# Kernel tuning notes

Measured on AMD Instinct MI355X. Metric: run time of the kernel, lower is better.

The kernel has to match this reference:

```python
import jax, jax.numpy as jnp
import numpy as np

C = 1024
H = C // 64          # 16 heads
CH = 64              # head dim
NUM_BUCKETS = 32
MAX_DISTANCE = 64
REL_SCALE = float(np.sqrt(CH))  # (channels//num_heads)**0.5 = 8
EPS = 1e-5


def group_norm(x, gamma, beta, groups):
    # x: [B, C, T]
    B, Cc, T = x.shape
    xg = x.reshape(B, groups, -1)
    m = xg.mean(-1, keepdims=True)
    v = xg.var(-1, keepdims=True)
    xn = ((xg - m) * jax.lax.rsqrt(v + EPS)).reshape(B, Cc, T)
    return xn * gamma[None, :, None] + beta[None, :, None]


def conv1d(x, w, b, pad):
    # x: [B, Cin, T], w: [Cout, Cin, K]
    y = jax.lax.conv_general_dilated(x, w, (1,), [(pad, pad)],
                                     dimension_numbers=('NCH', 'OIH', 'NCH'))
    return y + b[None, :, None]


def rel_pos_bias(T, emb):
    # lucidrains RelativePositionBias, non-causal; emb: [num_buckets, H]
    pos = jnp.arange(T)
    n = pos[:, None] - pos[None, :]          # n = -(k - q) = q - k
    half = NUM_BUCKETS // 2                  # 16
    ret = (n < 0).astype(jnp.int32) * half
    n = jnp.abs(n)
    max_exact = half // 2                    # 8
    is_small = n < max_exact
    nf = jnp.maximum(n, 1).astype(jnp.float32)
    val_large = max_exact + (jnp.log(nf / max_exact)
                             / np.log(MAX_DISTANCE / max_exact)
                             * (half - max_exact)).astype(jnp.int32)
    val_large = jnp.minimum(val_large, half - 1)
    bucket = ret + jnp.where(is_small, n, val_large)  # [T, T]
    return emb[bucket].transpose(2, 0, 1)             # [H, T, T]


def setup_inputs() -> dict:
    key = jax.random.key(0)
    ks = jax.random.split(key, 20)
    B, T = 8, 1024
    s = 0.02
    return {
        'x': jax.random.normal(ks[0], (B, C, T), jnp.float32),
        # ResBlock in_layers
        'rb_gn1_g': jnp.ones((C,), jnp.float32),
        'rb_gn1_b': jnp.zeros((C,), jnp.float32),
        'rb_conv1_w': jax.random.normal(ks[1], (C, C, 3), jnp.float32) * s,
        'rb_conv1_b': jnp.zeros((C,), jnp.float32),
        # ResBlock out_layers (zero-init in original; randomized for testing)
        'rb_gn2_g': jnp.ones((C,), jnp.float32),
        'rb_gn2_b': jnp.zeros((C,), jnp.float32),
        'rb_conv2_w': jax.random.normal(ks[2], (C, C, 3), jnp.float32) * s,
        'rb_conv2_b': jnp.zeros((C,), jnp.float32),
        # outer GroupNorm(8, C)
        'norm_g': jnp.ones((C,), jnp.float32),
        'norm_b': jnp.zeros((C,), jnp.float32),
        # AttentionBlock
        'attn_gn_g': jnp.ones((C,), jnp.float32),
        'attn_gn_b': jnp.zeros((C,), jnp.float32),
        'qkv_w': jax.random.normal(ks[3], (3 * C, C, 1), jnp.float32) * s,
        'qkv_b': jnp.zeros((3 * C,), jnp.float32),
        'proj_w': jax.random.normal(ks[4], (C, C, 1), jnp.float32) * s,
        'proj_b': jnp.zeros((C,), jnp.float32),
        'rel_emb': jax.random.normal(ks[5], (NUM_BUCKETS, H), jnp.float32) * s,
    }


def reference(x, rb_gn1_g, rb_gn1_b, rb_conv1_w, rb_conv1_b,
              rb_gn2_g, rb_gn2_b, rb_conv2_w, rb_conv2_b,
              norm_g, norm_b, attn_gn_g, attn_gn_b,
              qkv_w, qkv_b, proj_w, proj_b, rel_emb):
    B, Cc, T = x.shape
    # ResBlock: GN32 -> SiLU -> conv3 -> GN32 -> SiLU -> (dropout=0) -> conv3, + skip
    h = jax.nn.silu(group_norm(x, rb_gn1_g, rb_gn1_b, 32))
    h = conv1d(h, rb_conv1_w, rb_conv1_b, 1)
    h = jax.nn.silu(group_norm(h, rb_gn2_g, rb_gn2_b, 32))
    h = conv1d(h, rb_conv2_w, rb_conv2_b, 1)
    h = x + h
    # outer GroupNorm(8)
    h = group_norm(h, norm_g, norm_b, 8)
    # AttentionBlock with relative position bias
    xin = h
    qkv = conv1d(group_norm(h, attn_gn_g, attn_gn_b, 32), qkv_w, qkv_b, 0)
    # channel layout after reshape(bs*H, 3*ch, T): [H, 3, ch]
    qkv = qkv.reshape(B, H, 3, CH, T)
    q, k, v = qkv[:, :, 0], qkv[:, :, 1], qkv[:, :, 2]
    scale = CH ** -0.25
    w = jnp.einsum('bhct,bhcs->bhts', q * scale, k * scale)
    bias = rel_pos_bias(T, rel_emb) * REL_SCALE       # [H, T, T]
    w = jax.nn.softmax((w + bias[None]).astype(jnp.float32), axis=-1).astype(w.dtype)
    a = jnp.einsum('bhts,bhcs->bhct', w, v).reshape(B, Cc, T)
    return xin + conv1d(a, proj_w, proj_b, 0)
```

## Files before the change

### kernel.cpp

```cpp
#include <hip/hip_runtime.h>

typedef __attribute__((ext_vector_type(4))) float f32x4;
typedef __attribute__((ext_vector_type(8))) __bf16 bf16x8;
typedef __attribute__((ext_vector_type(4))) unsigned short us4;
typedef __attribute__((ext_vector_type(8))) unsigned short us8;

#define DEVI static __device__ __forceinline__

DEVI unsigned short f2bf(float f){
  union { float f; unsigned u; } x; x.f = f;
  unsigned r = x.u + 0x7fffu + ((x.u >> 16) & 1u);
  return (unsigned short)(r >> 16);
}
DEVI float bf2f(unsigned short h){
  union { unsigned u; float f; } x; x.u = ((unsigned)h) << 16;
  return x.f;
}

typedef __attribute__((address_space(1))) unsigned int gu32;
typedef __attribute__((address_space(3))) unsigned int lu32;
DEVI void gll16(const void* g, void* l){
  __builtin_amdgcn_global_load_lds((gu32*)g, (lu32*)l, 16, 0, 0);
}

DEVI f32x4 mfma16(bf16x8 a, bf16x8 b, f32x4 c){
  return __builtin_amdgcn_mfma_f32_16x16x32_bf16(a, b, c, 0, 0, 0);
}

DEVI float wredsum(float v){
  #pragma unroll
  for (int m = 1; m < 64; m <<= 1) v += __shfl_xor(v, m);
  return v;
}

__global__ __launch_bounds__(256) void conv_w_prep2(const float* __restrict__ w1,
                                                    const float* __restrict__ w2,
                                                    unsigned short* __restrict__ wp1,
                                                    unsigned short* __restrict__ wp2){
  int idx = blockIdx.x * 256 + threadIdx.x;
  int sel = idx >> 20;
  int lo  = idx & 1048575;
  const float* p = (sel ? w2 : w1) + (size_t)lo * 3;
  unsigned short* wp = sel ? wp2 : wp1;
  wp[lo]           = f2bf(p[0]);
  wp[1048576 + lo] = f2bf(p[1]);
  wp[2097152 + lo] = f2bf(p[2]);
}

__global__ __launch_bounds__(256) void cast_f2b2(const float* __restrict__ qw,
                                                 const float* __restrict__ pw,
                                                 unsigned short* __restrict__ qo,
                                                 unsigned short* __restrict__ po){
  int idx = blockIdx.x * 256 + threadIdx.x;
  const float* src; unsigned short* dst; int lo;
  if (idx < 786432){ src = qw; dst = qo; lo = idx; }
  else             { src = pw; dst = po; lo = idx - 786432; }
  f32x4 v = *(const f32x4*)&src[(size_t)lo * 4];
  us4 o;
  #pragma unroll
  for (int j = 0; j < 4; j++) o[j] = f2bf(v[j]);
  *(us4*)&dst[(size_t)lo * 4] = o;
}

__global__ __launch_bounds__(256) void misc_prep(unsigned short* __restrict__ h1p,
                                                 unsigned short* __restrict__ g2p,
                                                 const float* __restrict__ emb,
                                                 float* __restrict__ btab){
  int bid = blockIdx.x;
  if (bid < 64){
    int idx = bid * 256 + threadIdx.x;
    int b = idx >> 11, rr = (idx >> 10) & 1, c = idx & 1023;
    size_t off = ((size_t)b * 1026 + (rr ? 1025 : 0)) * 1024 + c;
    h1p[off] = 0; g2p[off] = 0;
  } else {
    int idx = (bid - 64) * 256 + threadIdx.x;
    if (idx >= 2047 * 16) return;
    int d = idx >> 4, h = idx & 15;
    int n0 = d - 1023;
    int ret = (n0 < 0) ? 16 : 0;
    int n = (n0 < 0) ? -n0 : n0;
    int bucket;
    if (n < 8) bucket = ret + n;
    else {
      float ratio = logf((float)n * 0.125f) / 2.0794415416798357f;
      int vl = 8 + (int)(ratio * 8.0f);
      bucket = ret + (vl < 15 ? vl : 15);
    }
    btab[h * 2048 + d] = emb[bucket * 16 + h] * 11.541560327111707f;
  }
}

__global__ __launch_bounds__(256) void gn_stats_cast(const float* __restrict__ in,
                                                     float2* __restrict__ st,
                                                     unsigned short* __restrict__ xb){
  const int g = blockIdx.x; const int tid = threadIdx.x;
  const float* p = in + (size_t)g * 32768;
  unsigned short* q = xb + (size_t)g * 32768;
  float s = 0.f, s2 = 0.f;
  for (int i = tid * 4; i < 32768; i += 1024){
    f32x4 v = *(const f32x4*)&p[i];
    us4 o;
    #pragma unroll
    for (int j = 0; j < 4; j++){ s += v[j]; s2 += v[j] * v[j]; o[j] = f2bf(v[j]); }
    *(us4*)&q[i] = o;
  }
  s = wredsum(s); s2 = wredsum(s2);
  __shared__ float rs[4], rs2[4];
  if ((tid & 63) == 0){ rs[tid >> 6] = s; rs2[tid >> 6] = s2; }
  __syncthreads();
  if (tid == 0){
    float S = rs[0] + rs[1] + rs[2] + rs[3];
    float S2 = rs2[0] + rs2[1] + rs2[2] + rs2[3];
    float m = S * (1.f / 32768.f);
    float var = S2 * (1.f / 32768.f) - m * m;
    st[g] = make_float2(m, rsqrtf(var + 1e-5f));
  }
}

template<int SILU, int INBF16, int OUTPAD, int FROMPART>
__global__ __launch_bounds__(256) void gn_apply_tr(
    const void* __restrict__ inp, const float2* __restrict__ st,
    const float* __restrict__ gma, const float* __restrict__ bta,
    unsigned short* __restrict__ out)
{
  const int gid = blockIdx.x;
  const int tc = gid & 15, g = (gid >> 4) & 31, b = gid >> 9;
  const int tid = threadIdx.x;
  const int t0 = tc * 64;
  __shared__ __align__(16) unsigned short tr[64 * 40];
  float2 s;
  if (FROMPART){
    int g8 = g >> 2, k = g & 3;
    float S = 0.f, S2 = 0.f;
    #pragma unroll
    for (int j = 0; j < 4; j++){
      float2 v = st[(size_t)(b * 8 + g8) * 16 + k * 4 + j];
      S += v.x; S2 += v.y;
    }
    float m = S * (1.f / 32768.f);
    float var = S2 * (1.f / 32768.f) - m * m;
    s = make_float2(m, rsqrtf(var + 1e-5f));
  } else {
    s = st[b * 32 + g];
  }
  int c = tid >> 3, t8 = (tid & 7) * 8;
  int ch = g * 32 + c;
  float sc = gma[ch] * s.y;
  float sh = bta[ch] - s.x * sc;
  float vv[8];
  if (INBF16){
    const unsigned short* p = (const unsigned short*)inp + ((size_t)b * 1024 + ch) * 1024 + t0 + t8;
    us8 v = *(const us8*)p;
    #pragma unroll
    for (int j = 0; j < 8; j++) vv[j] = bf2f(v[j]);
  } else {
    const float* p = (const float*)inp + ((size_t)b * 1024 + ch) * 1024 + t0 + t8;
    f32x4 v0 = *(const f32x4*)p; f32x4 v1 = *(const f32x4*)(p + 4);
    #pragma unroll
    for (int j = 0; j < 4; j++){ vv[j] = v0[j]; vv[4 + j] = v1[j]; }
  }
  #pragma unroll
  for (int j = 0; j < 8; j++){
    float v = vv[j] * sc + sh;
    if (SILU) v = v / (1.f + __expf(-v));
    tr[(t8 + j) * 40 + c] = f2bf(v);
  }
  __syncthreads();
  int t = tid >> 2, c8 = (tid & 3) * 8;
  us8 d = *(const us8*)&tr[t * 40 + c8];
  size_t row = OUTPAD ? ((size_t)b * 1026 + 1 + t0 + t) : ((size_t)b * 1024 + t0 + t);
  *(us8*)&out[row * 1024 + g * 32 + c8] = d;
}

template<int SILU>
__global__ __launch_bounds__(256) void gn2_apply(const unsigned short* __restrict__ c1,
    const float2* __restrict__ part2, const float* __restrict__ gma, const float* __restrict__ bta,
    unsigned short* __restrict__ outp)
{
  const int tid = threadIdx.x;
  const int ck = blockIdx.x & 31, b = blockIdx.x >> 5;
  const int g = tid >> 3;
  float S = 0.f, S2 = 0.f;
  #pragma unroll
  for (int tt = 0; tt < 8; tt++){
    float2 v = part2[(size_t)(b * 8 + tt) * 32 + g];
    S += v.x; S2 += v.y;
  }
  float mm = S * (1.f / 32768.f);
  float var = S2 * (1.f / 32768.f) - mm * mm;
  float2 s = make_float2(mm, rsqrtf(var + 1e-5f));
  float sc[4], sh[4];
  #pragma unroll
  for (int j = 0; j < 4; j++){ int ch = tid * 4 + j; sc[j] = gma[ch] * s.y; sh[j] = bta[ch] - s.x * sc[j]; }
  const unsigned short* p = c1 + ((size_t)b * 1024 + ck * 32) * 1024 + tid * 4;
  unsigned short* q = outp + ((size_t)b * 1026 + 1 + ck * 32) * 1024 + tid * 4;
  for (int r = 0; r < 32; r++){
    us4 v = *(const us4*)&p[(size_t)r * 1024];
    us4 o;
    #pragma unroll
    for (int j = 0; j < 4; j++){
      float f = bf2f(v[j]) * sc[j] + sh[j];
      if (SILU) f = f / (1.f + __expf(-f));
      o[j] = f2bf(f);
    }
    *(us4*)&q[(size_t)r * 1024] = o;
  }
}

__global__ __launch_bounds__(256) void gn8_apply(const unsigned short* __restrict__ r,
    const float2* __restrict__ part8, const float* __restrict__ gma, const float* __restrict__ bta,
    unsigned short* __restrict__ xin, float2* __restrict__ part32){
  const int gid = blockIdx.x; const int tid = threadIdx.x;
  const int sub = gid & 15, g = (gid >> 4) & 7, b = gid >> 7;
  float S = 0.f, S2 = 0.f;
  #pragma unroll
  for (int tt = 0; tt < 8; tt++){
    float2 v = part8[(size_t)(b * 8 + tt) * 8 + g];
    S += v.x; S2 += v.y;
  }
  float mm = S * (1.f / 131072.f);
  float var = S2 * (1.f / 131072.f) - mm * mm;
  float2 s = make_float2(mm, rsqrtf(var + 1e-5f));
  const unsigned short* pr = r + ((size_t)(b * 8 + g)) * 131072 + sub * 8192;
  unsigned short* px = xin + ((size_t)(b * 8 + g)) * 131072 + sub * 8192;
  float ps = 0.f, ps2 = 0.f;
  for (int i = tid * 8; i < 8192; i += 2048){
    int c = g * 128 + sub * 8 + (i >> 10);
    float sc = gma[c] * s.y, sh = bta[c] - s.x * sc;
    us8 v = *(const us8*)&pr[i];
    us8 o;
    #pragma unroll
    for (int j = 0; j < 8; j++){
      float f = bf2f(v[j]) * sc + sh;
      ps += f; ps2 += f * f;
      o[j] = f2bf(f);
    }
    *(us8*)&px[i] = o;
  }
  ps = wredsum(ps); ps2 = wredsum(ps2);
  __shared__ float rs[4], rs2[4];
  if ((tid & 63) == 0){ rs[tid >> 6] = ps; rs2[tid >> 6] = ps2; }
  __syncthreads();
  if (tid == 0)
    part32[(size_t)(b * 8 + g) * 16 + sub] =
      make_float2(rs[0] + rs[1] + rs[2] + rs[3], rs2[0] + rs2[1] + rs2[2] + rs2[3]);
}

template<int KK, int EPI, int GPART>
__global__ __launch_bounds__(256, 2) void gemm_k(
    const unsigned short* __restrict__ inT,
    const unsigned short* __restrict__ W,
    const float* __restrict__ bias,
    void* __restrict__ outp,
    void* __restrict__ resp,
    float2* __restrict__ part,
    int OC, int NT)
{
  __shared__ __align__(16) unsigned short Alds[2][128 * 64];
  __shared__ __align__(16) unsigned short Blds[2][128 * 64];
  __shared__ float sred[16];
  const int tid = threadIdx.x;
  const int lane = tid & 63;
  const int w = tid >> 6;
  const int wn = w >> 1, wo = w & 1;
  const int nt = blockIdx.x % NT;
  const int ot = blockIdx.x / NT;
  const int b = nt >> 3;
  const int t0 = (nt & 7) * 128;
  const int ob = ot * 128;
  const int rowbase = (KK == 3) ? (b * 1026 + t0) : (b * 1024 + t0);
  const int NTI = KK * 16;

  f32x4 acc[4][4];
  #pragma unroll
  for (int m = 0; m < 4; m++)
    #pragma unroll
    for (int n = 0; n < 4; n++) acc[m][n] = 0.f;

  const int lrow = lane >> 3;
  const int lblk = lane & 7;

  auto stage = [&](int kt, int bufsel){
    int kk = kt >> 4;
    int i0 = (kt & 15) * 64;
    const unsigned short* Ab = inT + (size_t)(rowbase + kk) * 1024;
    const unsigned short* Bb = W + ((size_t)kk * OC + ob) * 1024;
    #pragma unroll
    for (int j = 0; j < 4; ++j){
      int chunk = w * 4 + j;
      int row = chunk * 8 + lrow;
      int gcol = (lblk ^ (row & 7)) * 8;
      gll16(Ab + (size_t)row * 1024 + i0 + gcol, &Alds[bufsel][chunk * 512]);
      gll16(Bb + (size_t)row * 1024 + i0 + gcol, &Blds[bufsel][chunk * 512]);
    }
  };

  stage(0, 0);
  stage(1, 1);
  asm volatile("s_waitcnt vmcnt(8)" ::: "memory");
  __builtin_amdgcn_sched_barrier(0);
  __builtin_amdgcn_s_barrier();
  __builtin_amdgcn_sched_barrier(0);

  #pragma unroll 2
  for (int kt = 0; kt < NTI; ++kt){
    const int cur = kt & 1;
    const unsigned short* Ab = &Alds[cur][0];
    const unsigned short* Bb = &Blds[cur][0];
    bf16x8 af[2][4], bfv[2][4];
    #pragma unroll
    for (int m = 0; m < 4; m++){
      int row = wn * 64 + m * 16 + (lane & 15);
      #pragma unroll
      for (int k2 = 0; k2 < 2; k2++){
        int blk = ((lane >> 4) + k2 * 4) ^ (row & 7);
        af[k2][m] = *(const bf16x8*)&Ab[row * 64 + blk * 8];
      }
    }
    #pragma unroll
    for (int n = 0; n < 4; n++){
      int row = wo * 64 + n * 16 + (lane & 15);
      #pragma unroll
      for (int k2 = 0; k2 < 2; k2++){
        int blk = ((lane >> 4) + k2 * 4) ^ (row & 7);
        bfv[k2][n] = *(const bf16x8*)&Bb[row * 64 + blk * 8];
      }
    }
    asm volatile("s_waitcnt lgkmcnt(0)" ::: "memory");
    __builtin_amdgcn_sched_barrier(0);
    __builtin_amdgcn_s_barrier();
    __builtin_amdgcn_sched_barrier(0);
    if (kt + 2 < NTI) stage(kt + 2, cur);
    __builtin_amdgcn_sched_barrier(0);
    __builtin_amdgcn_s_setprio(1);
    #pragma unroll
    for (int k2 = 0; k2 < 2; k2++)
      #pragma unroll
      for (int m = 0; m < 4; m++)
        #pragma unroll
        for (int n = 0; n < 4; n++)
          acc[m][n] = mfma16(af[k2][m], bfv[k2][n], acc[m][n]);
    __builtin_amdgcn_s_setprio(0);
    __builtin_amdgcn_sched_barrier(0);
    if (kt + 2 < NTI){ asm volatile("s_waitcnt vmcnt(8)" ::: "memory"); }
    else             { asm volatile("s_waitcnt vmcnt(0)" ::: "memory"); }
    __builtin_amdgcn_sched_barrier(0);
    __builtin_amdgcn_s_barrier();
    __builtin_amdgcn_sched_barrier(0);
  }

  if (EPI == 0){
    unsigned short* out = (unsigned short*)outp;
    float ps[2] = {0.f, 0.f}, ps2[2] = {0.f, 0.f};
    #pragma unroll
    for (int m = 0; m < 4; m++){
      int tl = t0 + wn * 64 + m * 16 + ((lane >> 4) * 4);
      #pragma unroll
      for (int n = 0; n < 4; n++){
        int o = ob + wo * 64 + n * 16 + (lane & 15);
        float bz = bias[o];
        size_t base = ((size_t)b * 1024 + tl) * OC + o;
        #pragma unroll
        for (int r = 0; r < 4; r++){
          float v = acc[m][n][r] + bz;
          if (GPART == 2){ ps[n >> 1] += v; ps2[n >> 1] += v * v; }
          out[base + (size_t)r * OC] = f2bf(v);
        }
      }
    }
    if (GPART == 2){
      #pragma unroll
      for (int j = 0; j < 2; j++){ ps[j] = wredsum(ps[j]); ps2[j] = wredsum(ps2[j]); }
      if (lane == 0){
        sred[w * 4 + 0] = ps[0]; sred[w * 4 + 1] = ps2[0];
        sred[w * 4 + 2] = ps[1]; sred[w * 4 + 3] = ps2[1];
      }
      __syncthreads();
      if (tid < 4){
        int g = tid, woo = g >> 1, jj = g & 1;
        float S  = sred[woo * 4 + jj * 2 + 0] + sred[(woo + 2) * 4 + jj * 2 + 0];
        float S2 = sred[woo * 4 + jj * 2 + 1] + sred[(woo + 2) * 4 + jj * 2 + 1];
        part[(size_t)(b * 8 + (nt & 7)) * 32 + ot * 4 + g] = make_float2(S, S2);
      }
    }
  } else if (EPI == 3){
    unsigned short* qkT = (unsigned short*)outp;
    unsigned short* vT  = (unsigned short*)resp;
    #pragma unroll
    for (int m = 0; m < 4; m++){
      int tl = t0 + wn * 64 + m * 16 + ((lane >> 4) * 4);
      #pragma unroll
      for (int n = 0; n < 4; n++){
        int o0 = ob + wo * 64 + n * 16;
        int h = o0 / 192;
        int rem0 = o0 - h * 192;
        int o = o0 + (lane & 15);
        float bz = bias[o];
        if (rem0 < 128){
          size_t base = ((size_t)b * 1024 + tl) * 2048 + h * 128 + rem0 + (lane & 15);
          #pragma unroll
          for (int r = 0; r < 4; r++)
            qkT[base + (size_t)r * 2048] = f2bf(acc[m][n][r] + bz);
        } else {
          int c = rem0 - 128 + (lane & 15);
          size_t base = (((size_t)(b * 16 + h)) * 64 + c) * 1024 + tl;
          us4 o4;
          #pragma unroll
          for (int r = 0; r < 4; r++) o4[r] = f2bf(acc[m][n][r] + bz);
          *(us4*)&vT[base] = o4;
        }
      }
    }
  } else if (EPI == 4){
    unsigned short* out = (unsigned short*)outp;
    const unsigned short* xr = (const unsigned short*)resp;
    float ps = 0.f, ps2 = 0.f;
    #pragma unroll
    for (int m = 0; m < 4; m++){
      int tl = t0 + wn * 64 + m * 16 + ((lane >> 4) * 4);
      #pragma unroll
      for (int n = 0; n < 4; n++){
        int o = ob + wo * 64 + n * 16 + (lane & 15);
        float bz = bias[o];
        size_t base = ((size_t)b * 1024 + o) * 1024 + tl;
        us4 xv = *(const us4*)&xr[base];
        us4 ov;
        #pragma unroll
        for (int r = 0; r < 4; r++){
          float v = bf2f(xv[r]) + acc[m][n][r] + bz;
          if (GPART == 8){ ps += v; ps2 += v * v; }
          ov[r] = f2bf(v);
        }
        *(us4*)&out[base] = ov;
      }
    }
    if (GPART == 8){
      ps = wredsum(ps); ps2 = wredsum(ps2);
      if (lane == 0){ sred[w * 2] = ps; sred[w * 2 + 1] = ps2; }
      __syncthreads();
      if (tid == 0){
        float S = sred[0] + sred[2] + sred[4] + sred[6];
        float S2 = sred[1] + sred[3] + sred[5] + sred[7];
        part[(size_t)(b * 8 + (nt & 7)) * 8 + ot] = make_float2(S, S2);
      }
    }
  } else {
    float* out = (float*)outp;
    #pragma unroll
    for (int m = 0; m < 4; m++){
      int tl = t0 + wn * 64 + m * 16 + ((lane >> 4) * 4);
      #pragma unroll
      for (int n = 0; n < 4; n++){
        int o = ob + wo * 64 + n * 16 + (lane & 15);
        float bz = bias[o];
        size_t base = ((size_t)b * 1024 + o) * 1024 + tl;
        const unsigned short* xr = (const unsigned short*)resp;
        us4 xv = *(const us4*)&xr[base];
        f32x4 v;
        v[0] = bf2f(xv[0]); v[1] = bf2f(xv[1]); v[2] = bf2f(xv[2]); v[3] = bf2f(xv[3]);
        #pragma unroll
        for (int r = 0; r < 4; r++) v[r] += acc[m][n][r] + bz;
        *(f32x4*)&out[base] = v;
      }
    }
  }
}

__global__ __launch_bounds__(256, 3) void attn_k9(
    const unsigned short* __restrict__ qkT,
    const unsigned short* __restrict__ vT,
    const float* __restrict__ btab,
    unsigned short* __restrict__ aT)
{
  __shared__ __align__(16) unsigned short Kb[2][64 * 64];
  __shared__ __align__(16) unsigned short Vb[2][64 * 64];
  __shared__ __align__(16) unsigned short Pb[4][32 * 64];
  __shared__ __align__(16) float cblds[288];
  const int tid = threadIdx.x, lane = tid & 63, w = tid >> 6;
  const int d0 = blockIdx.x;
  const int xcd = d0 & 7, slot = d0 >> 3;
  const int bh = xcd * 16 + (slot >> 3);
  const int qt = slot & 7;
  const int h = bh & 15, b = bh >> 4;
  const int q0b = qt * 128;
  const int q0 = q0b + w * 32;
  const unsigned short* qk = qkT + (size_t)b * 1024 * 2048 + h * 128;
  const unsigned short* vh = vT + ((size_t)(b * 16 + h)) * 64 * 1024;
  const int lc = lane & 15, lg = lane >> 4;

  const float bneg = btab[h * 2048 + 0];
  const float bpos = btab[h * 2048 + 2046];

  if (tid < 288) cblds[tid] = btab[h * 2048 + 879 + tid];

  bf16x8 qf[2][2];
  #pragma unroll
  for (int m = 0; m < 2; m++){
    const unsigned short* qrow = qk + (size_t)(q0 + m * 16 + lc) * 2048;
    #pragma unroll
    for (int k2 = 0; k2 < 2; k2++)
      qf[m][k2] = *(const bf16x8*)&qrow[k2 * 32 + lg * 8];
  }
  bf16x8 onesf;
  {
    us8 u;
    #pragma unroll
    for (int j = 0; j < 8; j++) u[j] = 0x3F80;
    onesf = *(bf16x8*)&u;
  }
  f32x4 oacc[2][4], lacc[2];
  #pragma unroll
  for (int m = 0; m < 2; m++){
    #pragma unroll
    for (int cb = 0; cb < 4; cb++) oacc[m][cb] = 0.f;
    lacc[m] = 0.f;
  }

  const int lr = lane >> 3, lb = lane & 7;
  const float qs = 0.18033688011112042f;

  #pragma unroll
  for (int j = 0; j < 2; j++){
    int chunk = w * 2 + j;
    int row = chunk * 8 + lr;
    int gcol = (lb ^ (row & 7)) * 8;
    gll16(qk + 64 + (size_t)row * 2048 + gcol, &Kb[0][chunk * 512]);
    gll16(vh + (size_t)row * 1024 + gcol, &Vb[0][chunk * 512]);
  }
  __syncthreads();

  for (int t = 0; t < 16; ++t){
    const int cur = t & 1;
    const int st0 = t * 64;
    if (t < 15){
      int nst = st0 + 64;
      #pragma unroll
      for (int j = 0; j < 2; j++){
        int chunk = w * 2 + j;
        int row = chunk * 8 + lr;
        int gcol = (lb ^ (row & 7)) * 8;
        gll16(qk + 64 + (size_t)(nst + row) * 2048 + gcol, &Kb[cur ^ 1][chunk * 512]);
        gll16(vh + (size_t)row * 1024 + nst + gcol, &Vb[cur ^ 1][chunk * 512]);
      }
    }
    f32x4 sfr[2][4];
    #pragma unroll
    for (int m = 0; m < 2; m++)
      #pragma unroll
      for (int sub = 0; sub < 4; sub++) sfr[m][sub] = 0.f;
    __builtin_amdgcn_s_setprio(1);
    #pragma unroll
    for (int sub = 0; sub < 4; sub++){
      int row = sub * 16 + lc;
      #pragma unroll
      for (int k2 = 0; k2 < 2; k2++){
        int blk = (lg + k2 * 4) ^ (row & 7);
        bf16x8 bk = *(const bf16x8*)&Kb[cur][row * 64 + blk * 8];
        sfr[0][sub] = mfma16(bk, qf[0][k2], sfr[0][sub]);
        sfr[1][sub] = mfma16(bk, qf[1][k2], sfr[1][sub]);
      }
    }
    __builtin_amdgcn_s_setprio(0);
    const bool unineg = (st0 >= q0 + 81);
    const bool unipos = (st0 + 113 <= q0);
    if (unineg || unipos){
      const float bc = unineg ? bneg : bpos;
      #pragma unroll
      for (int m = 0; m < 2; m++)
        #pragma unroll
        for (int sub = 0; sub < 4; sub++)
          #pragma unroll
          for (int r = 0; r < 4; r++)
            sfr[m][sub][r] = exp2f(fmaf(sfr[m][sub][r], qs, bc));
    } else {
      #pragma unroll
      for (int m = 0; m < 2; m++){
        const float* bp = &cblds[(q0 + m * 16 + lc) - st0 + 144 - lg * 4];
        #pragma unroll
        for (int sub = 0; sub < 4; sub++)
          #pragma unroll
          for (int r = 0; r < 4; r++)
            sfr[m][sub][r] = exp2f(fmaf(sfr[m][sub][r], qs, bp[-(sub * 16) - r]));
      }
    }
    unsigned short* P = &Pb[w][0];
    #pragma unroll
    for (int m = 0; m < 2; m++){
      int qrow = m * 16 + lc;
      int rsw = (qrow & 7) << 3;
      #pragma unroll
      for (int sub = 0; sub < 4; sub++){
        int col = sub * 16 + lg * 4;
        unsigned w0, w1;
        asm("v_cvt_pk_bf16_f32 %0, %1, %2" : "=v"(w0) : "v"(sfr[m][sub][0]), "v"(sfr[m][sub][1]));
        asm("v_cvt_pk_bf16_f32 %0, %1, %2" : "=v"(w1) : "v"(sfr[m][sub][2]), "v"(sfr[m][sub][3]));
        uint2 pk; pk.x = w0; pk.y = w1;
        *(uint2*)&P[qrow * 64 + (col ^ rsw)] = pk;
      }
    }
    __builtin_amdgcn_s_setprio(1);
    #pragma unroll
    for (int k2 = 0; k2 < 2; k2++){
      bf16x8 pa[2];
      #pragma unroll
      for (int m = 0; m < 2; m++){
        int rowp = m * 16 + lc;
        int blkp = (lg + k2 * 4) ^ (rowp & 7);
        pa[m] = *(const bf16x8*)&P[rowp * 64 + blkp * 8];
      }
      #pragma unroll
      for (int cb = 0; cb < 4; cb++){
        int ch = cb * 16 + lc;
        int blkv = (lg + k2 * 4) ^ (ch & 7);
        bf16x8 bv = *(const bf16x8*)&Vb[cur][ch * 64 + blkv * 8];
        oacc[0][cb] = mfma16(pa[0], bv, oacc[0][cb]);
        oacc[1][cb] = mfma16(pa[1], bv, oacc[1][cb]);
      }
      lacc[0] = mfma16(pa[0], onesf, lacc[0]);
      lacc[1] = mfma16(pa[1], onesf, lacc[1]);
    }
    __builtin_amdgcn_s_setprio(0);
    __syncthreads();
  }
  #pragma unroll
  for (int m = 0; m < 2; m++)
    #pragma unroll
    for (int r = 0; r < 4; r++){
      float li = 1.0f / lacc[m][r];
      int tq = q0 + m * 16 + lg * 4 + r;
      #pragma unroll
      for (int cb = 0; cb < 4; cb++){
        int ch = h * 64 + cb * 16 + lc;
        aT[((size_t)b * 1024 + tq) * 1024 + ch] = f2bf(oacc[m][cb][r] * li);
      }
    }
}

extern "C" void kernel_launch(void* const* d_in, const int* in_sizes, int n_in,
                              void* d_out, int out_size, void* d_ws, size_t ws_size,
                              hipStream_t stream)
{
  const float* x       = (const float*)d_in[0];
  const float* gn1_g   = (const float*)d_in[1];
  const float* gn1_b   = (const float*)d_in[2];
  const float* conv1_w = (const float*)d_in[3];
  const float* conv1_b = (const float*)d_in[4];
  const float* gn2_g   = (const float*)d_in[5];
  const float* gn2_b   = (const float*)d_in[6];
  const float* conv2_w = (const float*)d_in[7];
  const float* conv2_b = (const float*)d_in[8];
  const float* norm_g  = (const float*)d_in[9];
  const float* norm_b  = (const float*)d_in[10];
  const float* agn_g   = (const float*)d_in[11];
  const float* agn_b   = (const float*)d_in[12];
  const float* qkv_w   = (const float*)d_in[13];
  const float* qkv_b   = (const float*)d_in[14];
  const float* proj_w  = (const float*)d_in[15];
  const float* proj_b  = (const float*)d_in[16];
  const float* rel_emb = (const float*)d_in[17];

  if (ws_size < 139526144u) return;

  char* ws = (char*)d_ws;
  unsigned short* w1p   = (unsigned short*)(ws + 0);
  unsigned short* w2p   = (unsigned short*)(ws + 6291456);
  unsigned short* wqkv  = (unsigned short*)(ws + 12582912);
  unsigned short* wproj = (unsigned short*)(ws + 18874368);
  float* btab           = (float*)(ws + 20971520);
  float2* stats1        = (float2*)(ws + 21102592);
  float2* part2n        = (float2*)(ws + 21110784);
  float2* part8n        = (float2*)(ws + 21127168);
  float2* part32        = (float2*)(ws + 21131264);
  unsigned short* h1p   = (unsigned short*)(ws + 22020096);
  unsigned short* c1    = (unsigned short*)(ws + 38830080);
  unsigned short* g2p   = (unsigned short*)(ws + 55607296);
  unsigned short* qkT   = h1p;
  unsigned short* vT    = (unsigned short*)(ws + 55574528);
  unsigned short* xb    = (unsigned short*)(ws + 72417280);
  unsigned short* attn_in = (unsigned short*)(ws + 72417280);
  unsigned short* xin   = (unsigned short*)(ws + 105971712);
  unsigned short* aT    = (unsigned short*)(ws + 122748928);

  conv_w_prep2<<<8192, 256, 0, stream>>>(conv1_w, conv2_w, w1p, w2p);
  cast_f2b2<<<4096, 256, 0, stream>>>(qkv_w, proj_w, wqkv, wproj);
  misc_prep<<<192, 256, 0, stream>>>(h1p, g2p, rel_emb, btab);

  gn_stats_cast<<<256, 256, 0, stream>>>(x, stats1, xb);
  gn_apply_tr<1, 1, 1, 0><<<4096, 256, 0, stream>>>(xb, stats1, gn1_g, gn1_b, h1p);

  gemm_k<3, 0, 2><<<512, 256, 0, stream>>>(h1p, w1p, conv1_b, c1, nullptr, part2n, 1024, 64);
  gn2_apply<1><<<256, 256, 0, stream>>>(c1, part2n, gn2_g, gn2_b, g2p);

  gemm_k<3, 4, 8><<<512, 256, 0, stream>>>(g2p, w2p, conv2_b, xb, xb, part8n, 1024, 64);
  gn8_apply<<<1024, 256, 0, stream>>>(xb, part8n, norm_g, norm_b, xin, part32);

  gn_apply_tr<0, 1, 0, 1><<<4096, 256, 0, stream>>>(xin, part32, agn_g, agn_b, attn_in);

  gemm_k<1, 3, 0><<<1536, 256, 0, stream>>>(attn_in, wqkv, qkv_b, qkT, vT, nullptr, 3072, 64);

  attn_k9<<<1024, 256, 0, stream>>>(qkT, vT, btab, aT);

  gemm_k<1, 2, 0><<<512, 256, 0, stream>>>(aT, wproj, proj_b, d_out, xin, nullptr, 1024, 64);
}
```

Before: 336.3 us.

## Single-buffer K/V in attention with staggered async loads to raise occupancy

The attention kernel drops the double-buffered K and V LDS tiles in favour of single buffers, which cuts LDS per block, and raises launch bounds from 3 to 4 blocks per CU. To keep the loads overlapped, the next K tile is issued right after QK^T finishes reading K, and the next V tile after PV finishes, with explicit vmcnt waits and raw s_barriers in place of __syncthreads. The aim is more resident waves to hide latency. In exchange each iteration has more barriers, the load-to-use distance is shorter, and the tighter register budget may cause spills.

```diff
diff --git a/kernel.cpp b/kernel.cpp
--- a/kernel.cpp
+++ b/kernel.cpp
@@ -466,14 +466,14 @@
   }
 }
 
-__global__ __launch_bounds__(256, 3) void attn_k9(
+__global__ __launch_bounds__(256, 4) void attn_k10(
     const unsigned short* __restrict__ qkT,
     const unsigned short* __restrict__ vT,
     const float* __restrict__ btab,
     unsigned short* __restrict__ aT)
 {
-  __shared__ __align__(16) unsigned short Kb[2][64 * 64];
-  __shared__ __align__(16) unsigned short Vb[2][64 * 64];
+  __shared__ __align__(16) unsigned short Kb[64 * 64];
+  __shared__ __align__(16) unsigned short Vb[64 * 64];
   __shared__ __align__(16) unsigned short Pb[4][32 * 64];
   __shared__ __align__(16) float cblds[288];
   const int tid = threadIdx.x, lane = tid & 63, w = tid >> 6;
@@ -524,14 +524,37 @@
     int chunk = w * 2 + j;
     int row = chunk * 8 + lr;
     int gcol = (lb ^ (row & 7)) * 8;
-    gll16(qk + 64 + (size_t)row * 2048 + gcol, &Kb[0][chunk * 512]);
-    gll16(vh + (size_t)row * 1024 + gcol, &Vb[0][chunk * 512]);
-  }
-  __syncthreads();
+    gll16(qk + 64 + (size_t)row * 2048 + gcol, &Kb[chunk * 512]);
+    gll16(vh + (size_t)row * 1024 + gcol, &Vb[chunk * 512]);
+  }
+  asm volatile("s_waitcnt vmcnt(0)" ::: "memory");
+  __builtin_amdgcn_sched_barrier(0);
+  __builtin_amdgcn_s_barrier();
+  __builtin_amdgcn_sched_barrier(0);
 
   for (int t = 0; t < 16; ++t){
-    const int cur = t & 1;
     const int st0 = t * 64;
+    f32x4 sfr[2][4];
+    #pragma unroll
+    for (int m = 0; m < 2; m++)
+      #pragma unroll
+      for (int sub = 0; sub < 4; sub++) sfr[m][sub] = 0.f;
+    __builtin_amdgcn_s_setprio(1);
+    #pragma unroll
+    for (int sub = 0; sub < 4; sub++){
+      int row = sub * 16 + lc;
+      #pragma unroll
+      for (int k2 = 0; k2 < 2; k2++){
+        int blk = (lg + k2 * 4) ^ (row & 7);
+        bf16x8 bk = *(const bf16x8*)&Kb[row * 64 + blk * 8];
+        sfr[0][sub] = mfma16(bk, qf[0][k2], sfr[0][sub]);
+        sfr[1][sub] = mfma16(bk, qf[1][k2], sfr[1][sub]);
+      }
+    }
+    __builtin_amdgcn_s_setprio(0);
+    __builtin_amdgcn_sched_barrier(0);
+    __builtin_amdgcn_s_barrier();
+    __builtin_amdgcn_sched_barrier(0);
     if (t < 15){
       int nst = st0 + 64;
       #pragma unroll
@@ -539,28 +562,10 @@
         int chunk = w * 2 + j;
         int row = chunk * 8 + lr;
         int gcol = (lb ^ (row & 7)) * 8;
-        gll16(qk + 64 + (size_t)(nst + row) * 2048 + gcol, &Kb[cur ^ 1][chunk * 512]);
-        gll16(vh + (size_t)row * 1024 + nst + gcol, &Vb[cur ^ 1][chunk * 512]);
-      }
-    }
-    f32x4 sfr[2][4];
-    #pragma unroll
-    for (int m = 0; m < 2; m++)
-      #pragma unroll
-      for (int sub = 0; sub < 4; sub++) sfr[m][sub] = 0.f;
-    __builtin_amdgcn_s_setprio(1);
-    #pragma unroll
-    for (int sub = 0; sub < 4; sub++){
-      int row = sub * 16 + lc;
-      #pragma unroll
-      for (int k2 = 0; k2 < 2; k2++){
-        int blk = (lg + k2 * 4) ^ (row & 7);
-        bf16x8 bk = *(const bf16x8*)&Kb[cur][row * 64 + blk * 8];
-        sfr[0][sub] = mfma16(bk, qf[0][k2], sfr[0][sub]);
-        sfr[1][sub] = mfma16(bk, qf[1][k2], sfr[1][sub]);
-      }
-    }
-    __builtin_amdgcn_s_setprio(0);
+        gll16(qk + 64 + (size_t)(nst + row) * 2048 + gcol, &Kb[chunk * 512]);
+      }
+    }
+    __builtin_amdgcn_sched_barrier(0);
     const bool unineg = (st0 >= q0 + 81);
     const bool unipos = (st0 + 113 <= q0);
     if (unineg || unipos){
@@ -598,6 +603,11 @@
         *(uint2*)&P[qrow * 64 + (col ^ rsw)] = pk;
       }
     }
+    if (t < 15){ asm volatile("s_waitcnt vmcnt(2)" ::: "memory"); }
+    else       { asm volatile("s_waitcnt vmcnt(0)" ::: "memory"); }
+    __builtin_amdgcn_sched_barrier(0);
+    __builtin_amdgcn_s_barrier();
+    __builtin_amdgcn_sched_barrier(0);
     __builtin_amdgcn_s_setprio(1);
     #pragma unroll
     for (int k2 = 0; k2 < 2; k2++){
@@ -612,7 +622,7 @@
       for (int cb = 0; cb < 4; cb++){
         int ch = cb * 16 + lc;
         int blkv = (lg + k2 * 4) ^ (ch & 7);
-        bf16x8 bv = *(const bf16x8*)&Vb[cur][ch * 64 + blkv * 8];
+        bf16x8 bv = *(const bf16x8*)&Vb[ch * 64 + blkv * 8];
         oacc[0][cb] = mfma16(pa[0], bv, oacc[0][cb]);
         oacc[1][cb] = mfma16(pa[1], bv, oacc[1][cb]);
       }
@@ -620,7 +630,23 @@
       lacc[1] = mfma16(pa[1], onesf, lacc[1]);
     }
     __builtin_amdgcn_s_setprio(0);
-    __syncthreads();
+    if (t < 15){
+      __builtin_amdgcn_sched_barrier(0);
+      __builtin_amdgcn_s_barrier();
+      __builtin_amdgcn_sched_barrier(0);
+      int nst = st0 + 64;
+      #pragma unroll
+      for (int j = 0; j < 2; j++){
+        int chunk = w * 2 + j;
+        int row = chunk * 8 + lr;
+        int gcol = (lb ^ (row & 7)) * 8;
+        gll16(vh + (size_t)row * 1024 + nst + gcol, &Vb[chunk * 512]);
+      }
+      asm volatile("s_waitcnt vmcnt(2)" ::: "memory");
+      __builtin_amdgcn_sched_barrier(0);
+      __builtin_amdgcn_s_barrier();
+      __builtin_amdgcn_sched_barrier(0);
+    }
   }
   #pragma unroll
   for (int m = 0; m < 2; m++)
@@ -698,7 +724,7 @@
 
   gemm_k<1, 3, 0><<<1536, 256, 0, stream>>>(attn_in, wqkv, qkv_b, qkT, vT, nullptr, 3072, 64);
 
-  attn_k9<<<1024, 256, 0, stream>>>(qkT, vT, btab, aT);
+  attn_k10<<<1024, 256, 0, stream>>>(qkT, vT, btab, aT);
 
   gemm_k<1, 2, 0><<<512, 256, 0, stream>>>(aT, wproj, proj_b, d_out, xin, nullptr, 1024, 64);
 }
```

Measured after the change: 361.9 us. +7.6%, slower.
